# Performance work log

Measured on AMD Instinct MI355X. Metric: run time of the kernel, lower is better.

## Reference

```python
import jax, jax.numpy as jnp
import numpy as np
import math

B, L, HID = 2, 1024, 768
H, TOPK = 12, 32
D = HID // H


def setup_inputs() -> dict:
    key = jax.random.key(0)
    ks = jax.random.split(key, 8)
    return {
        "hidden_states": jax.random.normal(ks[0], (B, L, HID), jnp.float32),
        "rel_bbox_emb": jax.random.normal(ks[1], (B, L, TOPK, HID), jnp.float32),
        "rel_bbox_index": jax.random.randint(ks[2], (B, L, TOPK), 0, L),
        "attention_mask": jnp.zeros((B, 1, L, L), jnp.bool_),
        "rel_pos": jax.random.normal(ks[3], (B, H, L, L), jnp.float32),
        "rel_2d_pos": jax.random.normal(ks[4], (B, H, L, L), jnp.float32),
        "w_qkv": jax.random.normal(ks[5], (HID, 3 * HID), jnp.float32) * (HID ** -0.5),
        "q_bias": jnp.zeros((HID,), jnp.float32),
        "v_bias": jnp.zeros((HID,), jnp.float32),
        "w_rq": jax.random.normal(ks[6], (HID, HID), jnp.float32) * (HID ** -0.5),
        "b_rq": jnp.zeros((HID,), jnp.float32),
    }


def _heads(x):  # [B,L,HID] -> [B,H,L,D]
    b, l, _ = x.shape
    return x.reshape(b, l, H, D).transpose(0, 2, 1, 3)


def reference(hidden_states, rel_bbox_emb, rel_bbox_index, attention_mask,
              rel_pos, rel_2d_pos, w_qkv, q_bias, v_bias, w_rq, b_rq):
    b, l, hid = hidden_states.shape
    scale = 1.0 / math.sqrt(D)
    NEG = jnp.float32(-1e8)

    qkv = hidden_states @ w_qkv                     # [B,L,3*HID]
    q, k, v = jnp.split(qkv, 3, axis=-1)
    q = q + q_bias
    v = v + v_bias

    ql = _heads(q) * scale                          # [B,H,L,D]
    kl = _heads(k)
    vl = _heads(v)
    scores = jnp.einsum('bhid,bhjd->bhij', ql, kl)  # [B,H,L,L]

    # relative bbox bias: q_bbox . rel_bbox_emb over top-k neighbors, scatter-added
    qb = _heads(q @ w_rq + b_rq) * scale            # [B,H,L,D]
    rbe = rel_bbox_emb.reshape(b, l, TOPK, H, D).transpose(0, 3, 1, 2, 4)  # [B,H,L,T,D]
    bbox_scores = jnp.einsum('bhid,bhijd->bhij', qb, rbe)  # [B,H,L,T]

    bi = jnp.arange(b)[:, None, None, None]
    hi = jnp.arange(H)[None, :, None, None]
    li = jnp.arange(l)[None, None, :, None]
    ji = rel_bbox_index[:, None, :, :]              # [B,1,L,T] broadcast over heads
    scores = scores.at[bi, hi, li, ji].add(bbox_scores)

    # local attention: mask out all positions NOT in the top-k neighbor set
    local_mask = jnp.ones((b, H, l, l), jnp.bool_).at[bi, hi, li, ji].set(False)
    scores = jnp.where(local_mask, NEG, scores)

    scores = scores + rel_pos + rel_2d_pos
    scores = jnp.where(attention_mask, NEG, scores)

    probs = jax.nn.softmax(scores, axis=-1)
    ctx = jnp.einsum('bhij,bhjd->bhid', probs, vl)  # [B,H,L,D]
    ctx = ctx.transpose(0, 2, 1, 3).reshape(b, l, hid)
    return ctx
```

## Files before the change

### kernel.cpp

```cpp
#include <hip/hip_runtime.h>
#include <hip/hip_bf16.h>
#include <math.h>

#define B_    2
#define L_    1024
#define H_    12
#define D_    64
#define HID_  768
#define TOPK_ 32
#define NEG_  (-100000000.0f)
#define KP_   2304

typedef __attribute__((ext_vector_type(8))) short short8;
typedef __attribute__((ext_vector_type(4))) short short4v;
typedef __attribute__((ext_vector_type(4))) float f32x4;

__device__ __forceinline__ void gload16(const void* g, void* l) {
    __builtin_amdgcn_global_load_lds((const __attribute__((address_space(1))) void*)g,
                                     (__attribute__((address_space(3))) void*)l, 16, 0, 0);
}

__global__ void prep_bias(const float* __restrict__ qb_,
                          const float* __restrict__ vb_,
                          float* __restrict__ biasq) {
    int n = blockIdx.x * 256 + threadIdx.x;
    if (n >= 3 * HID_) return;
    float v = 0.f;
    if (n < HID_) v = qb_[n];
    else if (n >= 2 * HID_) v = vb_[n - 2 * HID_];
    biasq[n] = v;
}

__global__ __launch_bounds__(256) void split_a(const float* __restrict__ src, int srcStride,
                                               __hip_bfloat16* __restrict__ dst) {
    int idx = blockIdx.x * 256 + threadIdx.x;
    int r = idx / 192, c4 = (idx - r * 192) * 4;
    const float4 x = *(const float4*)(src + (size_t)r * srcStride + c4);
    float xs[4] = {x.x, x.y, x.z, x.w};
    short4v h4, l4;
#pragma unroll
    for (int j = 0; j < 4; ++j) {
        __hip_bfloat16 h = __float2bfloat16(xs[j]);
        __hip_bfloat16 l = __float2bfloat16(xs[j] - __bfloat162float(h));
        h4[j] = *(short*)&h;
        l4[j] = *(short*)&l;
    }
    short* d = (short*)(dst + (size_t)r * KP_ + c4);
    *(short4v*)(d)         = h4;
    *(short4v*)(d + 768)   = h4;
    *(short4v*)(d + 1536)  = l4;
}

__global__ __launch_bounds__(256) void split_w(const float* __restrict__ src, int N,
                                               __hip_bfloat16* __restrict__ dst) {
    __shared__ float tile[32][33];
    const int n0 = blockIdx.x * 32, k0 = blockIdx.y * 32;
    const int tx = threadIdx.x & 31, ty = threadIdx.x >> 5;
#pragma unroll
    for (int p = 0; p < 4; ++p) {
        int r = p * 8 + ty;
        tile[r][tx] = src[(size_t)(k0 + r) * N + n0 + tx];
    }
    __syncthreads();
#pragma unroll
    for (int p = 0; p < 4; ++p) {
        int nl = p * 8 + ty;
        float xv = tile[tx][nl];
        __hip_bfloat16 h = __float2bfloat16(xv);
        __hip_bfloat16 l = __float2bfloat16(xv - __bfloat162float(h));
        size_t base = (size_t)(n0 + nl) * KP_ + k0 + tx;
        dst[base]        = h;
        dst[base + 768]  = l;
        dst[base + 1536] = h;
    }
}

template<int BM, int BN>
__global__ __launch_bounds__(256) void gemm_split(
    const __hip_bfloat16* __restrict__ A,
    const __hip_bfloat16* __restrict__ Bt,
    const float* __restrict__ bias,
    float* __restrict__ C, int ldc)
{
    constexpr int NT  = KP_ / 64;
    constexpr int ACH = BM / 32;
    constexpr int BCH = BN / 32;
    constexpr int MI  = BM / 32;
    constexpr int NI  = BN / 32;
    __shared__ __align__(16) char smem[(BM + BN) * 128];

    const int tid  = threadIdx.x;
    const int wid  = tid >> 6, lane = tid & 63;
    const int wr   = wid >> 1, wc = wid & 1;
    const int bm   = blockIdx.y * BM, bn = blockIdx.x * BN;
    const int r4   = lane >> 4, l15 = lane & 15;

    f32x4 acc[MI][NI];
#pragma unroll
    for (int mi = 0; mi < MI; ++mi)
#pragma unroll
        for (int ni = 0; ni < NI; ++ni) acc[mi][ni] = (f32x4){0.f, 0.f, 0.f, 0.f};

    const char* Ab  = (const char*)A;
    const char* Btb = (const char*)Bt;

    for (int kt = 0; kt < NT; ++kt) {
        __syncthreads();
#pragma unroll
        for (int c = 0; c < ACH; ++c) {
            int slot = c * 4096 + tid * 16;
            int R = slot >> 7, cb = (slot >> 4) & 7;
            const char* g = Ab + (size_t)(bm + R) * (KP_ * 2) + kt * 128 + ((cb ^ (R & 7)) << 4);
            gload16(g, smem + c * 4096 + wid * 1024);
        }
#pragma unroll
        for (int c = 0; c < BCH; ++c) {
            int slot = c * 4096 + tid * 16;
            int R = slot >> 7, cb = (slot >> 4) & 7;
            const char* g = Btb + (size_t)(bn + R) * (KP_ * 2) + kt * 128 + ((cb ^ (R & 7)) << 4);
            gload16(g, smem + BM * 128 + c * 4096 + wid * 1024);
        }
        __syncthreads();

#pragma unroll
        for (int kk = 0; kk < 2; ++kk) {
            short8 af[MI], bfv[NI];
#pragma unroll
            for (int mi = 0; mi < MI; ++mi) {
                int m_loc = wr * (BM / 2) + mi * 16 + l15;
                int off = (m_loc * 128 + kk * 64 + r4 * 16) ^ ((m_loc & 7) << 4);
                af[mi] = *(const short8*)(smem + off);
            }
#pragma unroll
            for (int ni = 0; ni < NI; ++ni) {
                int n_loc = wc * (BN / 2) + ni * 16 + l15;
                int off = BM * 128 + ((n_loc * 128 + kk * 64 + r4 * 16) ^ ((n_loc & 7) << 4));
                bfv[ni] = *(const short8*)(smem + off);
            }
#pragma unroll
            for (int mi = 0; mi < MI; ++mi)
#pragma unroll
                for (int ni = 0; ni < NI; ++ni)
                    acc[mi][ni] = __builtin_amdgcn_mfma_f32_16x16x32_bf16(
                        af[mi], bfv[ni], acc[mi][ni], 0, 0, 0);
        }
    }

#pragma unroll
    for (int mi = 0; mi < MI; ++mi) {
        int row = bm + wr * (BM / 2) + mi * 16 + r4 * 4;
#pragma unroll
        for (int ni = 0; ni < NI; ++ni) {
            int col = bn + wc * (BN / 2) + ni * 16 + l15;
            float bv = bias[col];
#pragma unroll
            for (int reg = 0; reg < 4; ++reg)
                C[(size_t)(row + reg) * ldc + col] = acc[mi][ni][reg] + bv;
        }
    }
}

__global__ __launch_bounds__(384) void attn_kernel(
    const float* __restrict__ qkv,
    const float* __restrict__ qb,
    const float* __restrict__ rbe,
    const int*   __restrict__ ridx,
    const unsigned char* __restrict__ amask,
    const float* __restrict__ rel_pos,
    const float* __restrict__ rel2d,
    float* __restrict__ out)
{
    const int bi = blockIdx.x;
    const int b = bi >> 10, i = bi & (L_ - 1);
    const int tid = threadIdx.x;
    const int h = tid >> 5, t = tid & 31;
    const float scale = 0.125f;

    __shared__ __align__(16) float sQ[HID_];
    __shared__ __align__(16) float sQb[HID_];
    __shared__ int   sIdx[TOPK_];
    __shared__ unsigned char sFirst[TOPK_];
    __shared__ unsigned char sMask[TOPK_];
    __shared__ float sRel[H_][TOPK_];
    __shared__ float sBbox[H_][TOPK_];
    __shared__ float sScore[H_][TOPK_];
    __shared__ float sProb[H_][TOPK_];

    {
        const float* qrow  = qkv + (size_t)bi * (3 * HID_);
        const float* qbrow = qb + (size_t)bi * HID_;
        for (int d = tid; d < HID_; d += 384) {
            sQ[d]  = qrow[d]  * scale;
            sQb[d] = qbrow[d] * scale;
        }
        if (tid < TOPK_) sIdx[tid] = ridx[bi * TOPK_ + tid];
    }
    __syncthreads();

    const int j = sIdx[t];

    {
        size_t ro = (((size_t)(b * H_ + h)) * L_ + i) * L_ + j;
        sRel[h][t] = rel_pos[ro] + rel2d[ro];
        if (tid < TOPK_) {
            int jj = sIdx[tid];
            sMask[tid] = amask[((size_t)b * L_ + i) * L_ + jj];
            unsigned char f = 1;
            for (int t2 = 0; t2 < tid; ++t2)
                if (sIdx[t2] == jj) { f = 0; break; }
            sFirst[tid] = f;
        }
    }

    {
        const float* rrow = rbe + ((size_t)bi * TOPK_ + t) * HID_ + h * D_;
        const float* krow = qkv + (size_t)(b * L_ + j) * (3 * HID_) + HID_ + h * D_;
        const float* qbh  = sQb + h * D_;
        const float* qh   = sQ + h * D_;
        float accB0 = 0.f, accB1 = 0.f, accB2 = 0.f, accB3 = 0.f;
        float accK0 = 0.f, accK1 = 0.f, accK2 = 0.f, accK3 = 0.f;
#pragma unroll
        for (int it = 0; it < 16; it += 4) {
            const float4 r0 = *(const float4*)(rrow + (it + 0) * 4);
            const float4 r1 = *(const float4*)(rrow + (it + 1) * 4);
            const float4 r2 = *(const float4*)(rrow + (it + 2) * 4);
            const float4 r3 = *(const float4*)(rrow + (it + 3) * 4);
            const float4 k0 = *(const float4*)(krow + (it + 0) * 4);
            const float4 k1 = *(const float4*)(krow + (it + 1) * 4);
            const float4 k2 = *(const float4*)(krow + (it + 2) * 4);
            const float4 k3 = *(const float4*)(krow + (it + 3) * 4);
            const float4 qb0 = *(const float4*)(qbh + (it + 0) * 4);
            const float4 qb1 = *(const float4*)(qbh + (it + 1) * 4);
            const float4 qb2 = *(const float4*)(qbh + (it + 2) * 4);
            const float4 qb3 = *(const float4*)(qbh + (it + 3) * 4);
            const float4 q0 = *(const float4*)(qh + (it + 0) * 4);
            const float4 q1 = *(const float4*)(qh + (it + 1) * 4);
            const float4 q2 = *(const float4*)(qh + (it + 2) * 4);
            const float4 q3 = *(const float4*)(qh + (it + 3) * 4);
            accB0 = fmaf(r0.x, qb0.x, fmaf(r0.y, qb0.y, fmaf(r0.z, qb0.z, fmaf(r0.w, qb0.w, accB0))));
            accB1 = fmaf(r1.x, qb1.x, fmaf(r1.y, qb1.y, fmaf(r1.z, qb1.z, fmaf(r1.w, qb1.w, accB1))));
            accB2 = fmaf(r2.x, qb2.x, fmaf(r2.y, qb2.y, fmaf(r2.z, qb2.z, fmaf(r2.w, qb2.w, accB2))));
            accB3 = fmaf(r3.x, qb3.x, fmaf(r3.y, qb3.y, fmaf(r3.z, qb3.z, fmaf(r3.w, qb3.w, accB3))));
            accK0 = fmaf(k0.x, q0.x, fmaf(k0.y, q0.y, fmaf(k0.z, q0.z, fmaf(k0.w, q0.w, accK0))));
            accK1 = fmaf(k1.x, q1.x, fmaf(k1.y, q1.y, fmaf(k1.z, q1.z, fmaf(k1.w, q1.w, accK1))));
            accK2 = fmaf(k2.x, q2.x, fmaf(k2.y, q2.y, fmaf(k2.z, q2.z, fmaf(k2.w, q2.w, accK2))));
            accK3 = fmaf(k3.x, q3.x, fmaf(k3.y, q3.y, fmaf(k3.z, q3.z, fmaf(k3.w, q3.w, accK3))));
        }
        sBbox[h][t]  = (accB0 + accB1) + (accB2 + accB3);
        sScore[h][t] = (accK0 + accK1) + (accK2 + accK3) + sRel[h][t];
    }

    const int dd = (t) * 2;
    float2 vpre[TOPK_];
    {
        const float* vbase = qkv + (size_t)b * L_ * (3 * HID_) + 2 * HID_ + h * D_ + dd;
#pragma unroll
        for (int tt = 0; tt < TOPK_; ++tt)
            vpre[tt] = *(const float2*)(vbase + (size_t)sIdx[tt] * (3 * HID_));
    }
    __syncthreads();

    {
        float s = -INFINITY;
        if (sFirst[t]) {
            float bb = 0.f;
#pragma unroll
            for (int t2 = 0; t2 < TOPK_; ++t2)
                if (sIdx[t2] == j) bb += sBbox[h][t2];
            s = sScore[h][t] + bb;
            if (sMask[t]) s = NEG_;
        }
        float m = s;
        m = fmaxf(m, __shfl_xor(m, 1));  m = fmaxf(m, __shfl_xor(m, 2));
        m = fmaxf(m, __shfl_xor(m, 4));  m = fmaxf(m, __shfl_xor(m, 8));
        m = fmaxf(m, __shfl_xor(m, 16));
        float e = expf(s - m);
        float sum = e;
        sum += __shfl_xor(sum, 1);  sum += __shfl_xor(sum, 2);
        sum += __shfl_xor(sum, 4);  sum += __shfl_xor(sum, 8);
        sum += __shfl_xor(sum, 16);
        sProb[h][t] = e / sum;
    }
    __syncthreads();

    {
        float a0 = 0.f, a1 = 0.f;
#pragma unroll
        for (int tt = 0; tt < TOPK_; ++tt) {
            float p = sProb[h][tt];
            a0 = fmaf(p, vpre[tt].x, a0);
            a1 = fmaf(p, vpre[tt].y, a1);
        }
        float2 o; o.x = a0; o.y = a1;
        *(float2*)(out + (size_t)bi * HID_ + h * D_ + dd) = o;
    }
}

extern "C" void kernel_launch(void* const* d_in, const int* in_sizes, int n_in,
                              void* d_out, int out_size, void* d_ws, size_t ws_size,
                              hipStream_t stream)
{
    const float* hidden  = (const float*)d_in[0];
    const float* rbe     = (const float*)d_in[1];
    const int*   ridx    = (const int*)d_in[2];
    const unsigned char* amask = (const unsigned char*)d_in[3];
    const float* rel_pos = (const float*)d_in[4];
    const float* rel2d   = (const float*)d_in[5];
    const float* w_qkv   = (const float*)d_in[6];
    const float* q_bias  = (const float*)d_in[7];
    const float* v_bias  = (const float*)d_in[8];
    const float* w_rq    = (const float*)d_in[9];
    const float* b_rq    = (const float*)d_in[10];
    float* out = (float*)d_out;

    const int M = B_ * L_;
    char* ws = (char*)d_ws;
    float* qkv   = (float*)(ws);
    float* qb    = (float*)(ws + 18874368);
    float* biasq = (float*)(ws + 25165824);
    __hip_bfloat16* A1  = (__hip_bfloat16*)(ws + 25175040);
    __hip_bfloat16* A2  = (__hip_bfloat16*)(ws + 34612224);
    __hip_bfloat16* Bt1 = (__hip_bfloat16*)(ws + 44049408);
    __hip_bfloat16* Bt2 = (__hip_bfloat16*)(ws + 54666240);

    prep_bias<<<9, 256, 0, stream>>>(q_bias, v_bias, biasq);
    split_a<<<1536, 256, 0, stream>>>(hidden, HID_, A1);
    split_w<<<dim3(2304 / 32, 768 / 32), 256, 0, stream>>>(w_qkv, 3 * HID_, Bt1);
    split_w<<<dim3(768 / 32, 768 / 32), 256, 0, stream>>>(w_rq, HID_, Bt2);

    gemm_split<128, 64><<<dim3((3 * HID_) / 64, M / 128), 256, 0, stream>>>(
        A1, Bt1, biasq, qkv, 3 * HID_);

    split_a<<<1536, 256, 0, stream>>>(qkv, 3 * HID_, A2);

    gemm_split<64, 64><<<dim3(HID_ / 64, M / 64), 256, 0, stream>>>(
        A2, Bt2, b_rq, qb, HID_);

    attn_kernel<<<B_ * L_, 384, 0, stream>>>(qkv, qb, rbe, ridx, amask,
                                             rel_pos, rel2d, out);
}
```

Before: 542.2 us.

## Vectorize weight split stores, defer V gathers, raise attn occupancy, widen QKV GEMM tile

The weight split kernel now has each thread convert four consecutive k values and write them as 4-wide short vectors, replacing scattered 2-byte stores. The attention kernel no longer holds 32 float2 V values in registers across the softmax. It gathers V in chunks of 8 inside the output loop and adds a launch_bounds occupancy hint of 6 to cut register pressure. The QKV GEMM switches to 128x128 tiles, which halves the block count and may reduce occupancy or leave CUs idle. Moving the V loads later also stops them from overlapping with the softmax, so their latency is exposed.

```diff
diff --git a/kernel.cpp b/kernel.cpp
--- a/kernel.cpp
+++ b/kernel.cpp
@@ -62,17 +62,21 @@
         tile[r][tx] = src[(size_t)(k0 + r) * N + n0 + tx];
     }
     __syncthreads();
-#pragma unroll
-    for (int p = 0; p < 4; ++p) {
-        int nl = p * 8 + ty;
-        float xv = tile[tx][nl];
+    const int kg = threadIdx.x & 7;
+    const int nl = threadIdx.x >> 3;
+    short4v h4, l4;
+#pragma unroll
+    for (int e = 0; e < 4; ++e) {
+        float xv = tile[kg * 4 + e][nl];
         __hip_bfloat16 h = __float2bfloat16(xv);
         __hip_bfloat16 l = __float2bfloat16(xv - __bfloat162float(h));
-        size_t base = (size_t)(n0 + nl) * KP_ + k0 + tx;
-        dst[base]        = h;
-        dst[base + 768]  = l;
-        dst[base + 1536] = h;
-    }
+        h4[e] = *(short*)&h;
+        l4[e] = *(short*)&l;
+    }
+    short* d = (short*)(dst + (size_t)(n0 + nl) * KP_ + k0 + kg * 4);
+    *(short4v*)(d)        = h4;
+    *(short4v*)(d + 768)  = l4;
+    *(short4v*)(d + 1536) = h4;
 }
 
 template<int BM, int BN>
@@ -160,7 +164,7 @@
     }
 }
 
-__global__ __launch_bounds__(384) void attn_kernel(
+__global__ __launch_bounds__(384, 6) void attn_kernel(
     const float* __restrict__ qkv,
     const float* __restrict__ qb,
     const float* __restrict__ rbe,
@@ -249,15 +253,6 @@
         sBbox[h][t]  = (accB0 + accB1) + (accB2 + accB3);
         sScore[h][t] = (accK0 + accK1) + (accK2 + accK3) + sRel[h][t];
     }
-
-    const int dd = (t) * 2;
-    float2 vpre[TOPK_];
-    {
-        const float* vbase = qkv + (size_t)b * L_ * (3 * HID_) + 2 * HID_ + h * D_ + dd;
-#pragma unroll
-        for (int tt = 0; tt < TOPK_; ++tt)
-            vpre[tt] = *(const float2*)(vbase + (size_t)sIdx[tt] * (3 * HID_));
-    }
     __syncthreads();
 
     {
@@ -284,12 +279,21 @@
     __syncthreads();
 
     {
+        const int dd = t * 2;
+        const float* vbase = qkv + (size_t)b * L_ * (3 * HID_) + 2 * HID_ + h * D_ + dd;
         float a0 = 0.f, a1 = 0.f;
 #pragma unroll
-        for (int tt = 0; tt < TOPK_; ++tt) {
-            float p = sProb[h][tt];
-            a0 = fmaf(p, vpre[tt].x, a0);
-            a1 = fmaf(p, vpre[tt].y, a1);
+        for (int base = 0; base < TOPK_; base += 8) {
+            float2 v[8];
+#pragma unroll
+            for (int u = 0; u < 8; ++u)
+                v[u] = *(const float2*)(vbase + (size_t)sIdx[base + u] * (3 * HID_));
+#pragma unroll
+            for (int u = 0; u < 8; ++u) {
+                float p = sProb[h][base + u];
+                a0 = fmaf(p, v[u].x, a0);
+                a1 = fmaf(p, v[u].y, a1);
+            }
         }
         float2 o; o.x = a0; o.y = a1;
         *(float2*)(out + (size_t)bi * HID_ + h * D_ + dd) = o;
@@ -328,7 +332,7 @@
     split_w<<<dim3(2304 / 32, 768 / 32), 256, 0, stream>>>(w_qkv, 3 * HID_, Bt1);
     split_w<<<dim3(768 / 32, 768 / 32), 256, 0, stream>>>(w_rq, HID_, Bt2);
 
-    gemm_split<128, 64><<<dim3((3 * HID_) / 64, M / 128), 256, 0, stream>>>(
+    gemm_split<128, 128><<<dim3((3 * HID_) / 128, M / 128), 256, 0, stream>>>(
         A1, Bt1, biasq, qkv, 3 * HID_);
 
     split_a<<<1536, 256, 0, stream>>>(qkv, 3 * HID_, A2);
```

Measured after the change: 559.6 us. 3.2% more time.
